# Performance work log

Hardware: AMD Instinct MI355X
Metric: run time of the kernel (lower is better)

## Reference

```python
import jax, jax.numpy as jnp
import numpy as np
from jax import lax

BN_EPS = 1e-4  # both BatchNorm2d (epsilon=0.0001) and BatchNorm1d (eps=0.0001)


def bin_act(x):
    # deterministic 1-bit activation: 2*round(clamp((x+1)/2,0,1)) - 1
    return 2.0 * jnp.round(jnp.clip((x + 1.0) * 0.5, 0.0, 1.0)) - 1.0


def bin_w(w):
    # H = 1.0: wb = (round(clamp((w+1)/2,0,1))*2 - 1) * 1.0  -> values in {-1,+1}
    return 2.0 * jnp.round(jnp.clip((w + 1.0) * 0.5, 0.0, 1.0)) - 1.0


def conv3x3(x, w, b):
    # NCHW input, OIHW weight, stride 1, padding 1 (SAME for 3x3)
    y = lax.conv_general_dilated(x, bin_w(w), (1, 1), ((1, 1), (1, 1)),
                                 dimension_numbers=('NCHW', 'OIHW', 'NCHW'))
    return y + b[None, :, None, None]


def maxpool2(x):
    return lax.reduce_window(x, -jnp.inf, lax.max, (1, 1, 2, 2), (1, 1, 2, 2), 'VALID')


def bn2d(x, g, b):
    # training-mode BatchNorm2d: batch stats over (N,H,W), biased variance
    m = jnp.mean(x, axis=(0, 2, 3), keepdims=True)
    v = jnp.mean(jnp.square(x - m), axis=(0, 2, 3), keepdims=True)
    return (x - m) * lax.rsqrt(v + BN_EPS) * g[None, :, None, None] + b[None, :, None, None]


def bn1d(x, g, b):
    m = jnp.mean(x, axis=0)
    v = jnp.mean(jnp.square(x - m), axis=0)
    return (x - m) * lax.rsqrt(v + BN_EPS) * g + b


def linear(x, w, b):
    return x @ bin_w(w).T + b


def setup_inputs() -> dict:
    key = jax.random.key(0)
    ks = jax.random.split(key, 16)
    d = {}
    d['x'] = jax.random.normal(ks[0], (256, 3, 32, 32), jnp.float32)
    conv_shapes = [(128, 3), (128, 128), (256, 128), (256, 256), (512, 256), (512, 512)]
    for i, (co, ci) in enumerate(conv_shapes, start=1):
        d[f'cw{i}'] = jax.random.normal(ks[i], (co, ci, 3, 3), jnp.float32)
        d[f'cb{i}'] = jax.random.normal(jax.random.fold_in(ks[i], 1), (co,), jnp.float32) * 0.01
        d[f'g{i}'] = jnp.ones((co,), jnp.float32)
        d[f'be{i}'] = jnp.zeros((co,), jnp.float32)
    fc_shapes = [(1024, 8192), (1024, 1024), (10, 1024)]
    for i, (fo, fi) in enumerate(fc_shapes, start=1):
        d[f'fw{i}'] = jax.random.normal(ks[6 + i], (fo, fi), jnp.float32)
        d[f'fb{i}'] = jax.random.normal(jax.random.fold_in(ks[6 + i], 1), (fo,), jnp.float32) * 0.01
        d[f'gf{i}'] = jnp.ones((fo,), jnp.float32)
        d[f'bef{i}'] = jnp.zeros((fo,), jnp.float32)
    return d


def reference(x, cw1, cb1, g1, be1, cw2, cb2, g2, be2, cw3, cb3, g3, be3,
              cw4, cb4, g4, be4, cw5, cb5, g5, be5, cw6, cb6, g6, be6,
              fw1, fb1, gf1, bef1, fw2, fb2, gf2, bef2, fw3, fb3, gf3, bef3):
    x = bin_act(bn2d(conv3x3(x, cw1, cb1), g1, be1))                 # [B,128,32,32]
    x = bin_act(bn2d(maxpool2(conv3x3(x, cw2, cb2)), g2, be2))       # [B,128,16,16]
    x = bin_act(bn2d(conv3x3(x, cw3, cb3), g3, be3))                 # [B,256,16,16]
    x = bin_act(bn2d(maxpool2(conv3x3(x, cw4, cb4)), g4, be4))       # [B,256,8,8]
    x = bin_act(bn2d(conv3x3(x, cw5, cb5), g5, be5))                 # [B,512,8,8]
    x = bin_act(bn2d(maxpool2(conv3x3(x, cw6, cb6)), g6, be6))       # [B,512,4,4]
    x = x.reshape(x.shape[0], -1)                                     # [B,8192]
    x = bin_act(bn1d(linear(x, fw1, fb1), gf1, bef1))                 # [B,1024]
    x = bin_act(bn1d(linear(x, fw2, fb2), gf2, bef2))                 # [B,1024]
    x = bn1d(linear(x, fw3, fb3), gf3, bef3)                          # [B,10]
    return x
```

## Files before the change

kernel.cpp:

```cpp
#include <hip/hip_runtime.h>

using u64 = unsigned long long;


__device__ __forceinline__ int bin01(float x) {
  float u = (x + 1.0f) * 0.5f;
  u = fminf(fmaxf(u, 0.0f), 1.0f);
  return rintf(u) != 0.0f;
}

__global__ void pack_conv_w(const float* __restrict__ w, u64* __restrict__ out,
                            int Cout, int Cin) {
  const int cqn = Cin >> 6;
  const int total = Cout * 9 * cqn;
  const int idx = blockIdx.x * 256 + threadIdx.x;
  if (idx >= total) return;
  int r = idx;
  const int q = r % cqn; r /= cqn;
  const int kx = r % 3; r /= 3;
  const int ky = r % 3;
  const int co = r / 3;
  u64 word = 0;
  for (int l = 0; l < 64; ++l) {
    const int ci = q * 64 + l;
    if (bin01(w[((size_t)(co * Cin + ci) * 3 + ky) * 3 + kx])) word |= (1ull << l);
  }
  out[idx] = word;
}

__global__ void pack_fc_w(const float* __restrict__ w, u64* __restrict__ out,
                          int Fi, int Fo) {
  const int fiq = Fi >> 6;
  const int total = Fo * fiq;
  const int idx = blockIdx.x * 256 + threadIdx.x;
  if (idx >= total) return;
  const int q = idx % fiq, o = idx / fiq;
  u64 word = 0;
  for (int l = 0; l < 64; ++l)
    if (bin01(w[(size_t)o * Fi + q * 64 + l])) word |= (1ull << l);
  out[idx] = word;
}

__global__ void pack_fc1_w(const float* __restrict__ w, u64* __restrict__ out) {
  const int idx = blockIdx.x * 256 + threadIdx.x;
  const int o = idx >> 7, q = idx & 127;
  const int hw = q >> 3, cq = q & 7;
  u64 word = 0;
  for (int l = 0; l < 64; ++l) {
    const int f = (cq * 64 + l) * 16 + hw;
    if (bin01(w[(size_t)o * 8192 + f])) word |= (1ull << l);
  }
  out[idx] = word;
}

__global__ void pack_w1f(const float* __restrict__ w1, float* __restrict__ w1f) {
  const int i = blockIdx.x * 256 + threadIdx.x;
  if (i < 3456) w1f[i] = bin01(w1[i]) ? 1.0f : -1.0f;
}

__device__ __forceinline__ void stage_image(const float* __restrict__ x, int n,
                                            float* __restrict__ xs, int nthreads,
                                            int t) {
  for (int idx = t; idx < 3 * 34 * 34; idx += nthreads) {
    const int ci = idx / 1156, rem = idx % 1156;
    const int hy = rem / 34, wx = rem % 34;
    float v = 0.0f;
    if (hy >= 1 && hy <= 32 && wx >= 1 && wx <= 32)
      v = x[(size_t)n * 3072 + ci * 1024 + (hy - 1) * 32 + (wx - 1)];
    xs[idx] = v;
  }
}

template <int PASS>
__global__ void conv1_eval(const float* __restrict__ x,
                           const float* __restrict__ w1f,
                           const float* __restrict__ cb,
                           const float* __restrict__ st,
                           float* __restrict__ BL) {
  const int blk = blockIdx.x;
  const int n = blk >> 2, q = blk & 3;
  const int t = threadIdx.x;
  __shared__ float xs[3 * 34 * 34];
  __shared__ float yl[256 * 8];
  __shared__ float rl[2 * 8 * 8];
  stage_image(x, n, xs, 256, t);
  __syncthreads();
  const int hw = q * 256 + t;
  const int h = hw >> 5, w = hw & 31;
  float win[27];
#pragma unroll
  for (int k = 0; k < 27; ++k) {
    const int ci = k / 9, dy = (k % 9) / 3, dx = k % 3;
    win[k] = xs[ci * 1156 + (h + dy) * 34 + (w + dx)];
  }
  for (int cc = 0; cc < 16; ++cc) {
    float y8[8];
#pragma unroll
    for (int j8 = 0; j8 < 8; ++j8) {
      const int c = cc * 8 + j8;
      const float* wp = w1f + c * 27;
      float acc = 0.0f;
#pragma unroll
      for (int k = 0; k < 27; ++k) acc = fmaf(wp[k], win[k], acc);
      float y = acc + cb[c];
      if (PASS) { const float d = y - st[2 * c]; y = d * d; }
      y8[j8] = y;
    }
    __syncthreads();
#pragma unroll
    for (int j8 = 0; j8 < 8; ++j8) yl[t * 8 + j8] = y8[j8];
    __syncthreads();
    if (t < 128) {
      const int L = t >> 6, j = (t >> 3) & 7, c8 = t & 7;
      float r = yl[(L * 128 + j) * 8 + c8];
      for (int i = 1; i < 16; ++i) r += yl[(L * 128 + i * 8 + j) * 8 + c8];
      rl[(L * 8 + c8) * 8 + j] = r;
    }
    __syncthreads();
    if (t < 16) {
      const int L = t >> 3, c8 = t & 7;
      const float* p = rl + (L * 8 + c8) * 8;
      const float s =
          ((p[0] + p[1]) + (p[2] + p[3])) + ((p[4] + p[5]) + (p[6] + p[7]));
      BL[((size_t)(n * 8) + (q * 2 + L)) * 128 + (cc * 8 + c8)] = s;
    }
  }
}

__global__ void conv1_comb2(const float* __restrict__ BL, float* __restrict__ st,
                            int pass) {
  const int c = threadIdx.x;
  if (c >= 128) return;
  float S = 0.0f;
  for (int n = 0; n < 256; ++n) {
    const float* L = BL + (size_t)n * 1024;
    const float l0 = L[0 * 128 + c], l1 = L[1 * 128 + c], l2 = L[2 * 128 + c],
                l3 = L[3 * 128 + c], l4 = L[4 * 128 + c], l5 = L[5 * 128 + c],
                l6 = L[6 * 128 + c], l7 = L[7 * 128 + c];
    const float Ln = ((l0 + l1) + (l2 + l3)) + ((l4 + l5) + (l6 + l7));
    S = (n == 0) ? Ln : (S + Ln);
  }
  if (pass == 0) st[2 * c] = S / 262144.0f;
  else           st[2 * c + 1] = 1.0f / sqrtf(S / 262144.0f + 1e-4f);
}

__global__ void conv1_binz(const float* __restrict__ x,
                           const float* __restrict__ w1f,
                           const float* __restrict__ cb,
                           const float* __restrict__ st,
                           const float* __restrict__ g,
                           const float* __restrict__ be,
                           u64* __restrict__ out) {
  const int blk = blockIdx.x;
  const int n = blk >> 2, q = blk & 3;
  const int t = threadIdx.x;
  __shared__ float xs[3 * 34 * 34];
  stage_image(x, n, xs, 256, t);
  __syncthreads();
  const int hw = q * 256 + t;
  const int h = hw >> 5, w = hw & 31;
  float win[27];
#pragma unroll
  for (int k = 0; k < 27; ++k) {
    const int ci = k / 9, dy = (k % 9) / 3, dx = k % 3;
    win[k] = xs[ci * 1156 + (h + dy) * 34 + (w + dx)];
  }
  u64 m0 = 0, m1 = 0;
  for (int c = 0; c < 128; ++c) {
    const float* wp = w1f + c * 27;
    float acc = 0.0f;
#pragma unroll
    for (int k = 0; k < 27; ++k) acc = fmaf(wp[k], win[k], acc);
    const float y = acc + cb[c];
    const float tv = ((y - st[2 * c]) * st[2 * c + 1]) * g[c] + be[c];
    const u64 bit = (u64)bin01(tv);
    if (c < 64) m0 |= bit << c;
    else        m1 |= bit << (c - 64);
  }
  u64* dst = out + ((size_t)(n * 1024 + hw)) * 2;
  dst[0] = m0;
  dst[1] = m1;
}

template <int CQ, int POOL, int H, int COUT, int NCPB>
__launch_bounds__(256, 4)
__global__ void conv_bin(const u64* __restrict__ xin, const u64* __restrict__ wpk,
                         short* __restrict__ pre) {
  constexpr int OH = H / POOL;
  constexpr int PLANE = OH * OH;
  constexpr int G = 256 / PLANE;
  constexpr int NE = POOL * POOL;
  constexpr int NW_ = H * H * CQ;
  constexpr int QC = (CQ > 4) ? 4 : CQ;
  constexpr int NQC = CQ / QC;
  const int n = blockIdx.x;
  const int t = threadIdx.x;
  __shared__ u64 xs[NW_];
  const u64* src = xin + (size_t)n * NW_;
  for (int i = t; i < NW_; i += 256) xs[i] = src[i];
  __syncthreads();
  const int cosub = t / PLANE;
  const int pos = t % PLANE;
  const int oh = pos / OH, ow = pos % OH;

  int pc[NCPB][NE];
#pragma unroll
  for (int cc = 0; cc < NCPB; ++cc)
#pragma unroll
    for (int e = 0; e < NE; ++e) pc[cc][e] = 0;

#pragma unroll
  for (int qc = 0; qc < NQC; ++qc) {
#pragma unroll
    for (int k = 0; k < 9; ++k) {
      const int dy = k / 3, dx = k % 3;
      u64 cw[NE][QC];
      bool cv[NE];
#pragma unroll
      for (int py = 0; py < POOL; ++py) {
#pragma unroll
        for (int px = 0; px < POOL; ++px) {
          const int hh = oh * POOL + py + dy - 1;
          const int ww = ow * POOL + px + dx - 1;
          const bool v = ((unsigned)hh < (unsigned)H) && ((unsigned)ww < (unsigned)H);
          const int e = py * POOL + px;
          cv[e] = v;
          const int base = v ? ((hh * H + ww) * CQ + qc * QC) : 0;
#pragma unroll
          for (int q = 0; q < QC; ++q) cw[e][q] = xs[base + q];
        }
      }
#pragma unroll
      for (int cc = 0; cc < NCPB; ++cc) {
        const int co = (blockIdx.y * NCPB + cc) * G + cosub;
        const u64* wp = wpk + ((size_t)co * 9 + k) * CQ + qc * QC;
        u64 w[QC];
#pragma unroll
        for (int q = 0; q < QC; ++q) w[q] = wp[q];
#pragma unroll
        for (int e = 0; e < NE; ++e) {
          int tp = 0;
#pragma unroll
          for (int q = 0; q < QC; ++q) tp += __popcll(cw[e][q] ^ w[q]);
          pc[cc][e] += cv[e] ? tp : 0;
        }
      }
    }
  }

  int vcnt[NE];
#pragma unroll
  for (int py = 0; py < POOL; ++py) {
#pragma unroll
    for (int px = 0; px < POOL; ++px) {
      int cvn = 0;
#pragma unroll
      for (int dy = 0; dy < 3; ++dy)
#pragma unroll
        for (int dx = 0; dx < 3; ++dx) {
          const int hh = oh * POOL + py + dy - 1, ww = ow * POOL + px + dx - 1;
          cvn += (((unsigned)hh < (unsigned)H) && ((unsigned)ww < (unsigned)H)) ? 1 : 0;
        }
      vcnt[py * POOL + px] = cvn;
    }
  }
#pragma unroll
  for (int cc = 0; cc < NCPB; ++cc) {
    const int co = (blockIdx.y * NCPB + cc) * G + cosub;
    int best = -1000000;
#pragma unroll
    for (int e = 0; e < NE; ++e) {
      const int dot = vcnt[e] * (CQ * 64) - 2 * pc[cc][e];
      best = dot > best ? dot : best;
    }
    pre[((size_t)(n * COUT + co) * OH + oh) * OH + ow] = (short)best;
  }
}

template <int PASS>
__device__ __forceinline__ float acc8(const short* __restrict__ p, float b, float m,
                                      int start, int len) {
  float r[8];
#pragma unroll
  for (int j = 0; j < 8; ++j) {
    float y = (float)p[start + j] + b;
    if (PASS) { const float d = y - m; y = d * d; }
    r[j] = y;
  }
  for (int i = 8; i < len; i += 8) {
#pragma unroll
    for (int j = 0; j < 8; ++j) {
      float y = (float)p[start + i + j] + b;
      if (PASS) { const float d = y - m; y = d * d; }
      r[j] += y;
    }
  }
  return ((r[0] + r[1]) + (r[2] + r[3])) + ((r[4] + r[5]) + (r[6] + r[7]));
}

template <int PASS>
__device__ __forceinline__ float np_sum_hw(const short* __restrict__ p, float b,
                                           float m, int HW) {
  if (HW == 256) return acc8<PASS>(p, b, m, 0, 128) + acc8<PASS>(p, b, m, 128, 128);
  return acc8<PASS>(p, b, m, 0, HW);
}

template <int HW>
__global__ void conv_stats(const short* __restrict__ pre, const float* __restrict__ cb,
                           float* __restrict__ st, int Cout) {
  const int c = blockIdx.x;
  const int n = threadIdx.x;
  const float b = cb[c];
  const short* p = pre + ((size_t)n * Cout + c) * HW;
  __shared__ float ls[256];
  ls[n] = np_sum_hw<0>(p, b, 0.0f, HW);
  __syncthreads();
  __shared__ float ms;
  if (n == 0) {
    float S = ls[0];
    for (int i = 1; i < 256; ++i) S += ls[i];
    ms = S / (float)(256 * HW);
  }
  __syncthreads();
  const float m = ms;
  __syncthreads();
  ls[n] = np_sum_hw<1>(p, b, m, HW);
  __syncthreads();
  if (n == 0) {
    float S = ls[0];
    for (int i = 1; i < 256; ++i) S += ls[i];
    const float v = S / (float)(256 * HW);
    st[2 * c] = m;
    st[2 * c + 1] = 1.0f / sqrtf(v + 1e-4f);
  }
}

__global__ void bin2d(const short* __restrict__ pre, const float* __restrict__ st,
                      const float* __restrict__ cb, const float* __restrict__ g,
                      const float* __restrict__ be, u64* __restrict__ out,
                      int Cout, int OH) {
  const int CQ = Cout >> 6;
  const int HW = OH * OH;
  const int widx = blockIdx.x * 256 + threadIdx.x;
  const int hw = widx % HW;
  const int r = widx / HW;
  const int cq = r % CQ;
  const int n = r / CQ;
  const short* p = pre + ((size_t)(n * Cout + cq * 64)) * HW + hw;
  u64 mask = 0;
  for (int c = 0; c < 64; ++c) {
    const int ch = cq * 64 + c;
    const float val = (float)p[(size_t)c * HW] + cb[ch];
    const float tv = ((val - st[2 * ch]) * st[2 * ch + 1]) * g[ch] + be[ch];
    mask |= ((u64)bin01(tv)) << c;
  }
  out[((size_t)n * HW + hw) * CQ + cq] = mask;
}

__global__ void fc_layer(const u64* __restrict__ xin, const u64* __restrict__ wpk,
                         short* __restrict__ pre, int FiQ, int Fo) {
  const int o = blockIdx.x;
  const int n = threadIdx.x;
  const u64* xp = xin + (size_t)n * FiQ;
  const u64* wp = wpk + (size_t)o * FiQ;
  int pc = 0;
  for (int q = 0; q < FiQ; ++q) pc += __popcll(xp[q] ^ wp[q]);
  pre[(size_t)n * Fo + o] = (short)(FiQ * 64 - 2 * pc);
}

__global__ void fc_stats(const short* __restrict__ pre, const float* __restrict__ fb,
                         float* __restrict__ st, int Fo) {
  const int o = blockIdx.x * 256 + threadIdx.x;
  if (o >= Fo) return;
  const float b = fb[o];
  float S = (float)pre[o] + b;
  for (int n = 1; n < 256; ++n) S += (float)pre[(size_t)n * Fo + o] + b;
  const float m = S / 256.0f;
  float d0 = (float)pre[o] + b - m;
  float V = d0 * d0;
  for (int n = 1; n < 256; ++n) {
    const float d = (float)pre[(size_t)n * Fo + o] + b - m;
    V += d * d;
  }
  st[2 * o] = m;
  st[2 * o + 1] = 1.0f / sqrtf(V / 256.0f + 1e-4f);
}

__global__ void fc_bin(const short* __restrict__ pre, const float* __restrict__ st,
                       const float* __restrict__ fb, const float* __restrict__ g,
                       const float* __restrict__ be, u64* __restrict__ out, int Fo) {
  const int gid = blockIdx.x * 4 + (threadIdx.x >> 6);
  const int lane = threadIdx.x & 63;
  const int OQ = Fo >> 6;
  const int oq = gid % OQ, n = gid / OQ;
  const int o = oq * 64 + lane;
  const float val = (float)pre[(size_t)n * Fo + o] + fb[o];
  const float tv = ((val - st[2 * o]) * st[2 * o + 1]) * g[o] + be[o];
  const u64 mask = __ballot(bin01(tv));
  if (lane == 0) out[(size_t)n * OQ + oq] = mask;
}

__global__ void fc_out(const short* __restrict__ pre, const float* __restrict__ st,
                       const float* __restrict__ fb, const float* __restrict__ g,
                       const float* __restrict__ be, float* __restrict__ out) {
  const int i = blockIdx.x * 256 + threadIdx.x;
  if (i >= 2560) return;
  const int o = i % 10;
  const float val = (float)pre[i] + fb[o];
  out[i] = ((val - st[2 * o]) * st[2 * o + 1]) * g[o] + be[o];
}

extern "C" void kernel_launch(void* const* d_in, const int* in_sizes, int n_in,
                              void* d_out, int out_size, void* d_ws, size_t ws_size,
                              hipStream_t stream) {
  if (n_in < 37) return;
  const float* x = (const float*)d_in[0];
  const float *cw1 = (const float*)d_in[1],  *cb1 = (const float*)d_in[2],  *g1 = (const float*)d_in[3],  *be1 = (const float*)d_in[4];
  const float *cw2 = (const float*)d_in[5],  *cb2 = (const float*)d_in[6],  *g2 = (const float*)d_in[7],  *be2 = (const float*)d_in[8];
  const float *cw3 = (const float*)d_in[9],  *cb3 = (const float*)d_in[10], *g3 = (const float*)d_in[11], *be3 = (const float*)d_in[12];
  const float *cw4 = (const float*)d_in[13], *cb4 = (const float*)d_in[14], *g4 = (const float*)d_in[15], *be4 = (const float*)d_in[16];
  const float *cw5 = (const float*)d_in[17], *cb5 = (const float*)d_in[18], *g5 = (const float*)d_in[19], *be5 = (const float*)d_in[20];
  const float *cw6 = (const float*)d_in[21], *cb6 = (const float*)d_in[22], *g6 = (const float*)d_in[23], *be6 = (const float*)d_in[24];
  const float *fw1 = (const float*)d_in[25], *fb1 = (const float*)d_in[26], *gf1 = (const float*)d_in[27], *bef1 = (const float*)d_in[28];
  const float *fw2 = (const float*)d_in[29], *fb2 = (const float*)d_in[30], *gf2 = (const float*)d_in[31], *bef2 = (const float*)d_in[32];
  const float *fw3 = (const float*)d_in[33], *fb3 = (const float*)d_in[34], *gf3 = (const float*)d_in[35], *bef3 = (const float*)d_in[36];
  float* out = (float*)d_out;

  char* ws = (char*)d_ws;
  if (ws_size < 46137344) return;
  float* ST = (float*)ws;
  float* W1F = (float*)(ws + 32768);
  float* BL = (float*)(ws + 65536);
  u64* W = (u64*)(ws + 1179648);
  u64* A = (u64*)(ws + 2981888);
  short* PRE = (short*)(ws + 12582912);
  const int S1 = 0, S2 = 256, S3 = 512, S4 = 1024, S5 = 1536, S6 = 2560;
  const int SF1 = 3584, SF2 = 5632, SF3 = 7680;
  const size_t WC2 = 0, WC3 = 2304, WC4 = 6912, WC5 = 16128, WC6 = 34560;
  const size_t WF1 = 71424, WF2 = 202496, WF3 = 218880;
  const size_t A1 = 0, A2 = 524288, A3 = 655360, A4 = 917504, A5 = 983040;
  const size_t A6 = 1114112, AF1 = 1146880, AF2 = 1150976;

  pack_w1f<<<14, 256, 0, stream>>>(cw1, W1F);
  pack_conv_w<<<9, 256, 0, stream>>>(cw2, W + WC2, 128, 128);
  pack_conv_w<<<18, 256, 0, stream>>>(cw3, W + WC3, 256, 128);
  pack_conv_w<<<36, 256, 0, stream>>>(cw4, W + WC4, 256, 256);
  pack_conv_w<<<72, 256, 0, stream>>>(cw5, W + WC5, 512, 256);
  pack_conv_w<<<144, 256, 0, stream>>>(cw6, W + WC6, 512, 512);
  pack_fc1_w<<<512, 256, 0, stream>>>(fw1, W + WF1);
  pack_fc_w<<<64, 256, 0, stream>>>(fw2, W + WF2, 1024, 1024);
  pack_fc_w<<<1, 256, 0, stream>>>(fw3, W + WF3, 1024, 10);

  conv1_eval<0><<<1024, 256, 0, stream>>>(x, W1F, cb1, ST + S1, BL);
  conv1_comb2<<<1, 128, 0, stream>>>(BL, ST + S1, 0);
  conv1_eval<1><<<1024, 256, 0, stream>>>(x, W1F, cb1, ST + S1, BL);
  conv1_comb2<<<1, 128, 0, stream>>>(BL, ST + S1, 1);
  conv1_binz<<<1024, 256, 0, stream>>>(x, W1F, cb1, ST + S1, g1, be1, A + A1);

  conv_bin<2, 2, 32, 128, 4><<<dim3(256, 32), 256, 0, stream>>>(A + A1, W + WC2, PRE);
  conv_stats<256><<<128, 256, 0, stream>>>(PRE, cb2, ST + S2, 128);
  bin2d<<<512, 256, 0, stream>>>(PRE, ST + S2, cb2, g2, be2, A + A2, 128, 16);

  conv_bin<2, 1, 16, 256, 8><<<dim3(256, 32), 256, 0, stream>>>(A + A2, W + WC3, PRE);
  conv_stats<256><<<256, 256, 0, stream>>>(PRE, cb3, ST + S3, 256);
  bin2d<<<1024, 256, 0, stream>>>(PRE, ST + S3, cb3, g3, be3, A + A3, 256, 16);

  conv_bin<4, 2, 16, 256, 4><<<dim3(256, 16), 256, 0, stream>>>(A + A3, W + WC4, PRE);
  conv_stats<64><<<256, 256, 0, stream>>>(PRE, cb4, ST + S4, 256);
  bin2d<<<256, 256, 0, stream>>>(PRE, ST + S4, cb4, g4, be4, A + A4, 256, 8);

  conv_bin<4, 1, 8, 512, 8><<<dim3(256, 16), 256, 0, stream>>>(A + A4, W + WC5, PRE);
  conv_stats<64><<<512, 256, 0, stream>>>(PRE, cb5, ST + S5, 512);
  bin2d<<<512, 256, 0, stream>>>(PRE, ST + S5, cb5, g5, be5, A + A5, 512, 8);

  conv_bin<8, 2, 8, 512, 2><<<dim3(256, 16), 256, 0, stream>>>(A + A5, W + WC6, PRE);
  conv_stats<16><<<512, 256, 0, stream>>>(PRE, cb6, ST + S6, 512);
  bin2d<<<128, 256, 0, stream>>>(PRE, ST + S6, cb6, g6, be6, A + A6, 512, 4);

  fc_layer<<<1024, 256, 0, stream>>>(A + A6, W + WF1, PRE, 128, 1024);
  fc_stats<<<4, 256, 0, stream>>>(PRE, fb1, ST + SF1, 1024);
  fc_bin<<<1024, 256, 0, stream>>>(PRE, ST + SF1, fb1, gf1, bef1, A + AF1, 1024);

  fc_layer<<<1024, 256, 0, stream>>>(A + AF1, W + WF2, PRE, 16, 1024);
  fc_stats<<<4, 256, 0, stream>>>(PRE, fb2, ST + SF2, 1024);
  fc_bin<<<1024, 256, 0, stream>>>(PRE, ST + SF2, fb2, gf2, bef2, A + AF2, 1024);

  fc_layer<<<10, 256, 0, stream>>>(A + AF2, W + WF3, PRE, 16, 10);
  fc_stats<<<1, 256, 0, stream>>>(PRE, fb3, ST + SF3, 10);
  fc_out<<<10, 256, 0, stream>>>(PRE, ST + SF3, fb3, gf3, bef3, out);
}
```

Before: 1.138 ms.

## Compute BatchNorm variance in one pass via sum and sum of squares

Replaces the two-pass mean-then-centered-variance computation with single-pass sum and sum-of-squares accumulation in conv1, the conv stats kernels and the FC stats kernel. Variance is then computed as E[y^2]-m^2 in double precision. This removes one full conv1 evaluation and its reduction launch, and halves reads of the pre-activation buffers. It risks precision loss from cancellation, which binarized outputs near thresholds may expose. The BL/QL buffers are moved to alias the PRE region.

```diff
diff --git a/kernel.cpp b/kernel.cpp
--- a/kernel.cpp
+++ b/kernel.cpp
@@ -1,6 +1,7 @@
 #include <hip/hip_runtime.h>
 
 using u64 = unsigned long long;
+using s64 = long long;
 
 
 __device__ __forceinline__ int bin01(float x) {
@@ -71,18 +72,17 @@
   }
 }
 
-template <int PASS>
 __global__ void conv1_eval(const float* __restrict__ x,
                            const float* __restrict__ w1f,
                            const float* __restrict__ cb,
-                           const float* __restrict__ st,
-                           float* __restrict__ BL) {
+                           float* __restrict__ BL, float* __restrict__ QL) {
   const int blk = blockIdx.x;
   const int n = blk >> 2, q = blk & 3;
   const int t = threadIdx.x;
   __shared__ float xs[3 * 34 * 34];
   __shared__ float yl[256 * 8];
   __shared__ float rl[2 * 8 * 8];
+  __shared__ float ql[2 * 8 * 8];
   stage_image(x, n, xs, 256, t);
   __syncthreads();
   const int hw = q * 256 + t;
@@ -102,9 +102,7 @@
       float acc = 0.0f;
 #pragma unroll
       for (int k = 0; k < 27; ++k) acc = fmaf(wp[k], win[k], acc);
-      float y = acc + cb[c];
-      if (PASS) { const float d = y - st[2 * c]; y = d * d; }
-      y8[j8] = y;
+      y8[j8] = acc + cb[c];
     }
     __syncthreads();
 #pragma unroll
@@ -112,26 +110,38 @@
     __syncthreads();
     if (t < 128) {
       const int L = t >> 6, j = (t >> 3) & 7, c8 = t & 7;
-      float r = yl[(L * 128 + j) * 8 + c8];
-      for (int i = 1; i < 16; ++i) r += yl[(L * 128 + i * 8 + j) * 8 + c8];
+      const float y0 = yl[(L * 128 + j) * 8 + c8];
+      float r = y0, qq = y0 * y0;
+      for (int i = 1; i < 16; ++i) {
+        const float yv = yl[(L * 128 + i * 8 + j) * 8 + c8];
+        r += yv;
+        qq += yv * yv;
+      }
       rl[(L * 8 + c8) * 8 + j] = r;
+      ql[(L * 8 + c8) * 8 + j] = qq;
     }
     __syncthreads();
     if (t < 16) {
       const int L = t >> 3, c8 = t & 7;
       const float* p = rl + (L * 8 + c8) * 8;
+      const float* pq = ql + (L * 8 + c8) * 8;
       const float s =
           ((p[0] + p[1]) + (p[2] + p[3])) + ((p[4] + p[5]) + (p[6] + p[7]));
-      BL[((size_t)(n * 8) + (q * 2 + L)) * 128 + (cc * 8 + c8)] = s;
-    }
-  }
-}
-
-__global__ void conv1_comb2(const float* __restrict__ BL, float* __restrict__ st,
-                            int pass) {
+      const float qs =
+          pq[0] + pq[1] + pq[2] + pq[3] + pq[4] + pq[5] + pq[6] + pq[7];
+      const size_t off = ((size_t)(n * 8) + (q * 2 + L)) * 128 + (cc * 8 + c8);
+      BL[off] = s;
+      QL[off] = qs;
+    }
+  }
+}
+
+__global__ void conv1_comb2(const float* __restrict__ BL, const float* __restrict__ QL,
+                            float* __restrict__ st) {
   const int c = threadIdx.x;
   if (c >= 128) return;
   float S = 0.0f;
+  double Q = 0.0;
   for (int n = 0; n < 256; ++n) {
     const float* L = BL + (size_t)n * 1024;
     const float l0 = L[0 * 128 + c], l1 = L[1 * 128 + c], l2 = L[2 * 128 + c],
@@ -139,9 +149,15 @@
                 l6 = L[6 * 128 + c], l7 = L[7 * 128 + c];
     const float Ln = ((l0 + l1) + (l2 + l3)) + ((l4 + l5) + (l6 + l7));
     S = (n == 0) ? Ln : (S + Ln);
-  }
-  if (pass == 0) st[2 * c] = S / 262144.0f;
-  else           st[2 * c + 1] = 1.0f / sqrtf(S / 262144.0f + 1e-4f);
+    const float* Lq = QL + (size_t)n * 1024;
+    Q += (double)Lq[0 * 128 + c] + Lq[1 * 128 + c] + Lq[2 * 128 + c] +
+         Lq[3 * 128 + c] + Lq[4 * 128 + c] + Lq[5 * 128 + c] +
+         Lq[6 * 128 + c] + Lq[7 * 128 + c];
+  }
+  const float m = S / 262144.0f;
+  const double v = Q / 262144.0 - (double)m * (double)m;
+  st[2 * c] = m;
+  st[2 * c + 1] = (float)(1.0 / sqrt(v + 1e-4));
 }
 
 __global__ void conv1_binz(const float* __restrict__ x,
@@ -277,32 +293,26 @@
   }
 }
 
-template <int PASS>
-__device__ __forceinline__ float acc8(const short* __restrict__ p, float b, float m,
-                                      int start, int len) {
+template <int HW>
+__device__ __forceinline__ float acc8q(const short* __restrict__ p, float b,
+                                       int start, float& qacc) {
+  constexpr int LEN = (HW < 128) ? HW : 128;
   float r[8];
 #pragma unroll
   for (int j = 0; j < 8; ++j) {
-    float y = (float)p[start + j] + b;
-    if (PASS) { const float d = y - m; y = d * d; }
+    const float y = (float)p[start + j] + b;
     r[j] = y;
-  }
-  for (int i = 8; i < len; i += 8) {
+    qacc += y * y;
+  }
+  for (int i = 8; i < LEN; i += 8) {
 #pragma unroll
     for (int j = 0; j < 8; ++j) {
-      float y = (float)p[start + i + j] + b;
-      if (PASS) { const float d = y - m; y = d * d; }
+      const float y = (float)p[start + i + j] + b;
       r[j] += y;
+      qacc += y * y;
     }
   }
   return ((r[0] + r[1]) + (r[2] + r[3])) + ((r[4] + r[5]) + (r[6] + r[7]));
-}
-
-template <int PASS>
-__device__ __forceinline__ float np_sum_hw(const short* __restrict__ p, float b,
-                                           float m, int HW) {
-  if (HW == 256) return acc8<PASS>(p, b, m, 0, 128) + acc8<PASS>(p, b, m, 128, 128);
-  return acc8<PASS>(p, b, m, 0, HW);
 }
 
 template <int HW>
@@ -313,25 +323,23 @@
   const float b = cb[c];
   const short* p = pre + ((size_t)n * Cout + c) * HW;
   __shared__ float ls[256];
-  ls[n] = np_sum_hw<0>(p, b, 0.0f, HW);
-  __syncthreads();
-  __shared__ float ms;
-  if (n == 0) {
-    float S = ls[0];
-    for (int i = 1; i < 256; ++i) S += ls[i];
-    ms = S / (float)(256 * HW);
-  }
-  __syncthreads();
-  const float m = ms;
-  __syncthreads();
-  ls[n] = np_sum_hw<1>(p, b, m, HW);
+  __shared__ float lq[256];
+  float qacc = 0.0f;
+  float S;
+  if (HW == 256) S = acc8q<256>(p, b, 0, qacc) + acc8q<256>(p, b, 128, qacc);
+  else           S = acc8q<HW>(p, b, 0, qacc);
+  ls[n] = S;
+  lq[n] = qacc;
   __syncthreads();
   if (n == 0) {
-    float S = ls[0];
-    for (int i = 1; i < 256; ++i) S += ls[i];
-    const float v = S / (float)(256 * HW);
+    float Sf = ls[0];
+    for (int i = 1; i < 256; ++i) Sf += ls[i];
+    double Q = 0.0;
+    for (int i = 0; i < 256; ++i) Q += (double)lq[i];
+    const float m = Sf / (float)(256 * HW);
+    const double v = Q / (double)(256 * HW) - (double)m * (double)m;
     st[2 * c] = m;
-    st[2 * c + 1] = 1.0f / sqrtf(v + 1e-4f);
+    st[2 * c + 1] = (float)(1.0 / sqrt(v + 1e-4));
   }
 }
 
@@ -373,17 +381,21 @@
   const int o = blockIdx.x * 256 + threadIdx.x;
   if (o >= Fo) return;
   const float b = fb[o];
-  float S = (float)pre[o] + b;
-  for (int n = 1; n < 256; ++n) S += (float)pre[(size_t)n * Fo + o] + b;
+  const int k0 = pre[o];
+  float S = (float)k0 + b;
+  s64 Sk = k0, Sk2 = (s64)k0 * k0;
+  for (int n = 1; n < 256; ++n) {
+    const int k = pre[(size_t)n * Fo + o];
+    S += (float)k + b;
+    Sk += k;
+    Sk2 += (s64)k * k;
+  }
   const float m = S / 256.0f;
-  float d0 = (float)pre[o] + b - m;
-  float V = d0 * d0;
-  for (int n = 1; n < 256; ++n) {
-    const float d = (float)pre[(size_t)n * Fo + o] + b - m;
-    V += d * d;
-  }
+  const double bd = (double)b;
+  const double v = ((double)Sk2 + 2.0 * bd * (double)Sk + 256.0 * bd * bd) / 256.0 -
+                   (double)m * (double)m;
   st[2 * o] = m;
-  st[2 * o + 1] = 1.0f / sqrtf(V / 256.0f + 1e-4f);
+  st[2 * o + 1] = (float)(1.0 / sqrt(v + 1e-4));
 }
 
 __global__ void fc_bin(const short* __restrict__ pre, const float* __restrict__ st,
@@ -428,12 +440,13 @@
 
   char* ws = (char*)d_ws;
   if (ws_size < 46137344) return;
-  float* ST = (float*)ws;
+  float* ST  = (float*)ws;
   float* W1F = (float*)(ws + 32768);
-  float* BL = (float*)(ws + 65536);
-  u64* W = (u64*)(ws + 1179648);
-  u64* A = (u64*)(ws + 2981888);
+  u64*   W   = (u64*)(ws + 1179648);
+  u64*   A   = (u64*)(ws + 2981888);
   short* PRE = (short*)(ws + 12582912);
+  float* BL  = (float*)(ws + 12582912);
+  float* QL  = (float*)(ws + 12582912 + 1048576);
   const int S1 = 0, S2 = 256, S3 = 512, S4 = 1024, S5 = 1536, S6 = 2560;
   const int SF1 = 3584, SF2 = 5632, SF3 = 7680;
   const size_t WC2 = 0, WC3 = 2304, WC4 = 6912, WC5 = 16128, WC6 = 34560;
@@ -451,10 +464,8 @@
   pack_fc_w<<<64, 256, 0, stream>>>(fw2, W + WF2, 1024, 1024);
   pack_fc_w<<<1, 256, 0, stream>>>(fw3, W + WF3, 1024, 10);
 
-  conv1_eval<0><<<1024, 256, 0, stream>>>(x, W1F, cb1, ST + S1, BL);
-  conv1_comb2<<<1, 128, 0, stream>>>(BL, ST + S1, 0);
-  conv1_eval<1><<<1024, 256, 0, stream>>>(x, W1F, cb1, ST + S1, BL);
-  conv1_comb2<<<1, 128, 0, stream>>>(BL, ST + S1, 1);
+  conv1_eval<<<1024, 256, 0, stream>>>(x, W1F, cb1, BL, QL);
+  conv1_comb2<<<1, 128, 0, stream>>>(BL, QL, ST + S1);
   conv1_binz<<<1024, 256, 0, stream>>>(x, W1F, cb1, ST + S1, g1, be1, A + A1);
 
   conv_bin<2, 2, 32, 128, 4><<<dim3(256, 32), 256, 0, stream>>>(A + A1, W + WC2, PRE);
```

New measurement: 1.185 ms (median of 2 runs). +4.2%, slower.
